# Optimization experiments

Measured on AMD Instinct MI355X. Metric: run time of the kernel, lower is better.

The kernel has to match this reference:

```python
import jax, jax.numpy as jnp
import numpy as np

D3D, D2D, DTEXT, DPROJ, SEQ_LEN = 256, 768, 3072, 3072, 256
B, S, T = 32, 256, 512


def setup_inputs() -> dict:
    key = jax.random.key(0)
    ks = jax.random.split(key, 9)
    s3 = 1.0 / np.sqrt(D3D)
    s2 = 1.0 / np.sqrt(D2D)
    sf = 1.0 / np.sqrt(DPROJ * 3)
    return {
        "feat_3d": jax.random.normal(ks[0], (B, D3D), jnp.float32),
        "feat_2d": jax.random.normal(ks[1], (B, S, D2D), jnp.float32),
        "feat_text": jax.random.normal(ks[2], (B, T, DTEXT), jnp.float32),
        "W3d": jax.random.uniform(ks[3], (DPROJ, D3D), jnp.float32, -s3, s3),
        "b3d": jax.random.uniform(ks[4], (DPROJ,), jnp.float32, -s3, s3),
        "W2d": jax.random.uniform(ks[5], (DPROJ, D2D), jnp.float32, -s2, s2),
        "b2d": jax.random.uniform(ks[6], (DPROJ,), jnp.float32, -s2, s2),
        "Wf": jax.random.uniform(ks[7], (DPROJ, DPROJ * 3), jnp.float32, -sf, sf),
        "bf": jax.random.uniform(ks[8], (DPROJ,), jnp.float32, -sf, sf),
    }


def reference(feat_3d, feat_2d, feat_text, W3d, b3d, W2d, b2d, Wf, bf):
    # Projections
    f3p = feat_3d @ W3d.T + b3d                      # [B, P]
    f2p = jnp.einsum("bsd,pd->bsp", feat_2d, W2d) + b2d  # [B, S, P]

    # Attention pooling of 2D slice features against global 3D feature
    scores_s = jnp.einsum("bsp,bp->bs", f2p, f3p)    # [B, S]
    w_s = jax.nn.softmax(scores_s, axis=1)
    pooled_2d = jnp.einsum("bs,bsp->bp", w_s, f2p)   # [B, P]

    # Attention pooling of text features against global 3D feature
    scores_t = jnp.einsum("btp,bp->bt", feat_text, f3p)  # [B, T]
    w_t = jax.nn.softmax(scores_t, axis=1)
    pooled_text = jnp.einsum("bt,btp->bp", w_t, feat_text)  # [B, P]

    # All seq_len rows of the original's concatenated input are identical,
    # so compute the fusion GEMM once per batch element and broadcast.
    fused_vec = jnp.concatenate([f3p, pooled_2d, pooled_text], axis=-1) @ Wf.T + bf  # [B, P]
    return jnp.broadcast_to(fused_vec[:, None, :], (fused_vec.shape[0], SEQ_LEN, fused_vec.shape[1]))
```

## Files before the change

### kernel.cpp

```cpp
#include <hip/hip_runtime.h>

#define NB 32
#define NS 256
#define NT 512
#define KD3 256
#define KD2 768
#define NP 3072
#define KFZ 9216

__device__ __forceinline__ float wave_red_sum(float v) {
#pragma unroll
  for (int o = 32; o; o >>= 1) v += __shfl_xor(v, o, 64);
  return v;
}
__device__ __forceinline__ float wave_red_max(float v) {
#pragma unroll
  for (int o = 32; o; o >>= 1) v = fmaxf(v, __shfl_xor(v, o, 64));
  return v;
}

__global__ __launch_bounds__(256) void k1_f3p(const float* __restrict__ f3d,
                                              const float* __restrict__ W3d,
                                              const float* __restrict__ b3d,
                                              float* __restrict__ c0, float* __restrict__ c1,
                                              float* __restrict__ c2, float* __restrict__ c3) {
  int b = blockIdx.x & 31, pc = blockIdx.x >> 5;
  __shared__ float4 xs[KD3 / 4];
  int tid = threadIdx.x;
  if (tid < KD3 / 4) xs[tid] = ((const float4*)(f3d + b * KD3))[tid];
  __syncthreads();
  int p = pc * 256 + tid;
  const float4* wrow = (const float4*)(W3d + (size_t)p * KD3);
  float acc = b3d[p];
#pragma unroll 8
  for (int i = 0; i < KD3 / 4; ++i) {
    float4 w = wrow[i], x = xs[i];
    acc = fmaf(w.x, x.x, acc); acc = fmaf(w.y, x.y, acc);
    acc = fmaf(w.z, x.z, acc); acc = fmaf(w.w, x.w, acc);
  }
  size_t o = (size_t)b * KFZ + p;
  c0[o] = acc; c1[o] = 0.f; c2[o] = 0.f; c3[o] = 0.f;
}

__global__ __launch_bounds__(256, 2) void kT_text(const float* __restrict__ ftx,
                                                  const float* __restrict__ c0,
                                                  float* __restrict__ Pt,
                                                  float* __restrict__ ml) {
  int b = blockIdx.x & 31, tch = blockIdx.x >> 5;
  __shared__ float4 f4[NP / 4];
  int tid = threadIdx.x;
#pragma unroll
  for (int i = 0; i < 3; ++i)
    f4[tid + 256 * i] = ((const float4*)(c0 + (size_t)b * KFZ))[tid + 256 * i];
  __syncthreads();
  int wave = tid >> 6, lane = tid & 63;
  int t0 = tch * 32 + wave * 8;
  const float4* rbase = (const float4*)(ftx + ((size_t)(b * NT + t0)) * NP);
  float4 xa[12], xb[12];
#pragma unroll
  for (int j = 0; j < 12; ++j) xa[j] = rbase[lane + 64 * j];
  float m = -3.0e38f, l = 0.f;
  float4 acc[12];
#pragma unroll
  for (int j = 0; j < 12; ++j) acc[j] = make_float4(0.f, 0.f, 0.f, 0.f);
#pragma unroll
  for (int r = 0; r < 8; ++r) {
    float4* cur = (r & 1) ? xb : xa;
    float4* nxt = (r & 1) ? xa : xb;
    if (r < 7) {
      const float4* rn = rbase + (size_t)(r + 1) * (NP / 4);
#pragma unroll
      for (int j = 0; j < 12; ++j) nxt[j] = rn[lane + 64 * j];
    }
    float sx = 0.f, sy = 0.f, sz = 0.f, sw = 0.f;
#pragma unroll
    for (int j = 0; j < 12; ++j) {
      float4 f = f4[lane + 64 * j];
      sx = fmaf(cur[j].x, f.x, sx); sy = fmaf(cur[j].y, f.y, sy);
      sz = fmaf(cur[j].z, f.z, sz); sw = fmaf(cur[j].w, f.w, sw);
    }
    float s = (sx + sy) + (sz + sw);
    s = wave_red_sum(s);
    float mn = fmaxf(m, s);
    float al = __expf(m - mn);
    float e = __expf(s - mn);
    l = fmaf(l, al, e);
#pragma unroll
    for (int j = 0; j < 12; ++j) {
      acc[j].x = fmaf(acc[j].x, al, e * cur[j].x);
      acc[j].y = fmaf(acc[j].y, al, e * cur[j].y);
      acc[j].z = fmaf(acc[j].z, al, e * cur[j].z);
      acc[j].w = fmaf(acc[j].w, al, e * cur[j].w);
    }
    m = mn;
  }
  int c = tch * 4 + wave;
  float4* Pr = (float4*)(Pt + (size_t)(c * NB + b) * NP);
#pragma unroll
  for (int j = 0; j < 12; ++j) Pr[lane + 64 * j] = acc[j];
  if (lane == 0) { ml[(c * NB + b) * 2] = m; ml[(c * NB + b) * 2 + 1] = l; }
}

__global__ __launch_bounds__(256) void k2_gpart(const float* __restrict__ W2d,
                                                const float* __restrict__ c0,
                                                float* __restrict__ g_part) {
  int dc = blockIdx.x % 3, kc = blockIdx.x / 3;
  __shared__ float xs[NB * 96];
  int tid = threadIdx.x;
  int p0 = kc * 96;
  for (int i = tid; i < NB * 96; i += 256) {
    int bb = i / 96, pp = i - bb * 96;
    xs[i] = c0[(size_t)bb * KFZ + p0 + pp];
  }
  __syncthreads();
  int d = dc * 256 + tid;
  float acc[NB];
#pragma unroll
  for (int b = 0; b < NB; ++b) acc[b] = 0.f;
  for (int pp = 0; pp < 96; pp += 8) {
    float w[8];
#pragma unroll
    for (int u = 0; u < 8; ++u) w[u] = W2d[(size_t)(p0 + pp + u) * KD2 + d];
#pragma unroll
    for (int b = 0; b < NB; ++b) {
      float4 x0 = *(const float4*)&xs[b * 96 + pp];
      float4 x1 = *(const float4*)&xs[b * 96 + pp + 4];
      acc[b] = fmaf(w[0], x0.x, acc[b]); acc[b] = fmaf(w[1], x0.y, acc[b]);
      acc[b] = fmaf(w[2], x0.z, acc[b]); acc[b] = fmaf(w[3], x0.w, acc[b]);
      acc[b] = fmaf(w[4], x1.x, acc[b]); acc[b] = fmaf(w[5], x1.y, acc[b]);
      acc[b] = fmaf(w[6], x1.z, acc[b]); acc[b] = fmaf(w[7], x1.w, acc[b]);
    }
  }
#pragma unroll
  for (int b = 0; b < NB; ++b) g_part[(size_t)(kc * NB + b) * KD2 + d] = acc[b];
}

__global__ __launch_bounds__(256) void k3a_scores(const float* __restrict__ f2d,
                                                  const float* __restrict__ g_part,
                                                  float* __restrict__ sraw) {
  int b = blockIdx.x & 31, sc = blockIdx.x >> 5;
  __shared__ float4 g4[KD2 / 4];
  float* g = (float*)g4;
  int tid = threadIdx.x;
  for (int i = tid; i < KD2; i += 256) {
    float a = 0.f;
#pragma unroll 8
    for (int c = 0; c < 32; ++c) a += g_part[(size_t)(c * NB + b) * KD2 + i];
    g[i] = a;
  }
  __syncthreads();
  int wave = tid >> 6, lane = tid & 63;
#pragma unroll
  for (int grp = 0; grp < 2; ++grp) {
    int s0 = sc * 32 + wave * 8 + grp * 4;
    float4 x[4][3];
#pragma unroll
    for (int rr = 0; rr < 4; ++rr) {
      const float4* row = (const float4*)(f2d + ((size_t)b * NS + s0 + rr) * KD2);
#pragma unroll
      for (int j = 0; j < 3; ++j) x[rr][j] = row[lane + 64 * j];
    }
#pragma unroll
    for (int rr = 0; rr < 4; ++rr) {
      float acc = 0.f;
#pragma unroll
      for (int j = 0; j < 3; ++j) {
        float4 f = g4[lane + 64 * j];
        acc = fmaf(x[rr][j].x, f.x, acc); acc = fmaf(x[rr][j].y, f.y, acc);
        acc = fmaf(x[rr][j].z, f.z, acc); acc = fmaf(x[rr][j].w, f.w, acc);
      }
      acc = wave_red_sum(acc);
      if (lane == 0) sraw[b * NS + s0 + rr] = acc;
    }
  }
}

__global__ __launch_bounds__(256) void kComb(const float* __restrict__ Pt,
                                             const float* __restrict__ ml,
                                             float* __restrict__ c0, float* __restrict__ c1,
                                             float* __restrict__ c2, float* __restrict__ c3) {
  int b = blockIdx.x & 31, pc = blockIdx.x >> 5;
  __shared__ float sm[128];
  int tid = threadIdx.x;
  if (tid < 64) {
    sm[tid] = ml[(tid * NB + b) * 2];
    sm[64 + tid] = ml[(tid * NB + b) * 2 + 1];
  }
  __syncthreads();
  float M = -3.0e38f;
#pragma unroll 8
  for (int c = 0; c < 64; ++c) M = fmaxf(M, sm[c]);
  float denom = 0.f;
#pragma unroll 8
  for (int c = 0; c < 64; ++c) denom += __expf(sm[c] - M) * sm[64 + c];
  float inv = 1.f / denom;
  int p4 = pc * 1024 + tid * 4;
  float4 a = make_float4(0.f, 0.f, 0.f, 0.f);
#pragma unroll 2
  for (int cg = 0; cg < 8; ++cg) {
    float4 v[8];
#pragma unroll
    for (int u = 0; u < 8; ++u)
      v[u] = *(const float4*)&Pt[(size_t)((cg * 8 + u) * NB + b) * NP + p4];
#pragma unroll
    for (int u = 0; u < 8; ++u) {
      float w = __expf(sm[cg * 8 + u] - M);
      a.x = fmaf(w, v[u].x, a.x); a.y = fmaf(w, v[u].y, a.y);
      a.z = fmaf(w, v[u].z, a.z); a.w = fmaf(w, v[u].w, a.w);
    }
  }
  a.x *= inv; a.y *= inv; a.z *= inv; a.w *= inv;
  size_t o = (size_t)b * KFZ + 2 * NP + p4;
  float4 z = make_float4(0.f, 0.f, 0.f, 0.f);
  *(float4*)&c0[o] = a;
  *(float4*)&c1[o] = z; *(float4*)&c2[o] = z; *(float4*)&c3[o] = z;
}

__global__ __launch_bounds__(256) void k3c_sm(const float* __restrict__ f2d,
                                              const float* __restrict__ sraw,
                                              float* __restrict__ p2f) {
  int b = blockIdx.x & 31;
  int r = blockIdx.x >> 5;
  int dc = r % 3, sc = r / 3;
  __shared__ float pr[NS];
  __shared__ float red[8];
  int tid = threadIdx.x;
  int wave = tid >> 6, lane = tid & 63;
  float v = sraw[b * NS + tid];
  float mx = wave_red_max(v);
  if (lane == 0) red[wave] = mx;
  __syncthreads();
  float M = fmaxf(fmaxf(red[0], red[1]), fmaxf(red[2], red[3]));
  float e = __expf(v - M);
  pr[tid] = e;
  float smv = wave_red_sum(e);
  if (lane == 0) red[4 + wave] = smv;
  __syncthreads();
  float inv = 1.f / (red[4] + red[5] + red[6] + red[7]);
  int d = dc * 256 + tid;
  float acc = 0.f;
  const float* base = f2d + ((size_t)b * NS + sc * 64) * KD2 + d;
#pragma unroll 2
  for (int sg = 0; sg < 8; ++sg) {
    float xv[8];
#pragma unroll
    for (int u = 0; u < 8; ++u) xv[u] = base[(size_t)(sg * 8 + u) * KD2];
#pragma unroll
    for (int u = 0; u < 8; ++u) acc = fmaf(pr[sc * 64 + sg * 8 + u], xv[u], acc);
  }
  p2f[(size_t)(sc * NB + b) * KD2 + d] = acc * inv;
}

__global__ __launch_bounds__(256) void k5_pool2d(const float* __restrict__ W2d,
                                                 const float* __restrict__ b2d,
                                                 const float* __restrict__ p2f,
                                                 float* __restrict__ c0, float* __restrict__ c1,
                                                 float* __restrict__ c2, float* __restrict__ c3) {
  int pb = blockIdx.x >> 2, ks = blockIdx.x & 3;
  __shared__ __align__(16) float wt[64 * 68];
  __shared__ __align__(16) float xt[32 * 68];
  int tid = threadIdx.x;
  int tp = tid & 31, tb = tid >> 5;
  float acc[2][4];
#pragma unroll
  for (int i = 0; i < 2; ++i)
#pragma unroll
    for (int j = 0; j < 4; ++j) acc[i][j] = 0.f;
  for (int dk = 0; dk < 3; ++dk) {
    int d0 = ks * 192 + dk * 64;
#pragma unroll
    for (int it = 0; it < 4; ++it) {
      int idx = tid + it * 256;
      int row = idx >> 4, c4 = (idx & 15) * 4;
      *(float4*)&wt[row * 68 + c4] =
          *(const float4*)&W2d[(size_t)(pb * 64 + row) * KD2 + d0 + c4];
    }
#pragma unroll
    for (int it = 0; it < 2; ++it) {
      int idx = tid + it * 256;
      int row = idx >> 4, c4 = (idx & 15) * 4;
      float4 a = *(const float4*)&p2f[(size_t)row * KD2 + d0 + c4];
      float4 q1 = *(const float4*)&p2f[(size_t)(NB + row) * KD2 + d0 + c4];
      float4 q2 = *(const float4*)&p2f[(size_t)(2 * NB + row) * KD2 + d0 + c4];
      float4 q3 = *(const float4*)&p2f[(size_t)(3 * NB + row) * KD2 + d0 + c4];
      a.x += q1.x + q2.x + q3.x; a.y += q1.y + q2.y + q3.y;
      a.z += q1.z + q2.z + q3.z; a.w += q1.w + q2.w + q3.w;
      *(float4*)&xt[row * 68 + c4] = a;
    }
    __syncthreads();
#pragma unroll 4
    for (int kk = 0; kk < 64; kk += 4) {
      float4 wv[2], xv[4];
#pragma unroll
      for (int i = 0; i < 2; ++i) wv[i] = *(const float4*)&wt[(tp + 32 * i) * 68 + kk];
#pragma unroll
      for (int j = 0; j < 4; ++j) xv[j] = *(const float4*)&xt[(tb + 8 * j) * 68 + kk];
#pragma unroll
      for (int i = 0; i < 2; ++i)
#pragma unroll
        for (int j = 0; j < 4; ++j) {
          acc[i][j] = fmaf(wv[i].x, xv[j].x, acc[i][j]);
          acc[i][j] = fmaf(wv[i].y, xv[j].y, acc[i][j]);
          acc[i][j] = fmaf(wv[i].z, xv[j].z, acc[i][j]);
          acc[i][j] = fmaf(wv[i].w, xv[j].w, acc[i][j]);
        }
    }
    __syncthreads();
  }
  float* dst = (ks == 0) ? c0 : (ks == 1) ? c1 : (ks == 2) ? c2 : c3;
#pragma unroll
  for (int i = 0; i < 2; ++i) {
    int p = pb * 64 + tp + 32 * i;
    float bias = (ks == 0) ? b2d[p] : 0.f;
#pragma unroll
    for (int j = 0; j < 4; ++j)
      dst[(size_t)(tb + 8 * j) * KFZ + NP + p] = acc[i][j] + bias;
  }
}

__global__ __launch_bounds__(256) void k_csum(float* __restrict__ c0,
                                              const float* __restrict__ c1,
                                              const float* __restrict__ c2,
                                              const float* __restrict__ c3) {
  int i = blockIdx.x * 256 + threadIdx.x;
  float4 a = ((float4*)c0)[i];
  float4 v1 = ((const float4*)c1)[i];
  float4 v2 = ((const float4*)c2)[i];
  float4 v3 = ((const float4*)c3)[i];
  a.x += v1.x + v2.x + v3.x; a.y += v1.y + v2.y + v3.y;
  a.z += v1.z + v2.z + v3.z; a.w += v1.w + v2.w + v3.w;
  ((float4*)c0)[i] = a;
}

__global__ __launch_bounds__(256) void k6_fused(const float* __restrict__ Wf,
                                                const float* __restrict__ c0,
                                                float* __restrict__ fpart) {
  int pb = blockIdx.x >> 4, kc = blockIdx.x & 15;
  __shared__ __align__(16) float wt[96 * 68];
  __shared__ __align__(16) float xt[32 * 68];
  int tid = threadIdx.x;
  int tp = tid & 31, tb = tid >> 5;
  float acc[3][4];
#pragma unroll
  for (int i = 0; i < 3; ++i)
#pragma unroll
    for (int j = 0; j < 4; ++j) acc[i][j] = 0.f;
  for (int kt = 0; kt < 9; ++kt) {
    int k0 = kc * 576 + kt * 64;
#pragma unroll
    for (int it = 0; it < 6; ++it) {
      int idx = tid + it * 256;
      int row = idx >> 4, c4 = (idx & 15) * 4;
      *(float4*)&wt[row * 68 + c4] =
          *(const float4*)&Wf[(size_t)(pb * 96 + row) * KFZ + k0 + c4];
    }
#pragma unroll
    for (int it = 0; it < 2; ++it) {
      int idx = tid + it * 256;
      int row = idx >> 4, c4 = (idx & 15) * 4;
      *(float4*)&xt[row * 68 + c4] =
          *(const float4*)&c0[(size_t)row * KFZ + k0 + c4];
    }
    __syncthreads();
#pragma unroll 4
    for (int kk = 0; kk < 64; kk += 4) {
      float4 wv[3], xv[4];
#pragma unroll
      for (int i = 0; i < 3; ++i) wv[i] = *(const float4*)&wt[(tp + 32 * i) * 68 + kk];
#pragma unroll
      for (int j = 0; j < 4; ++j) xv[j] = *(const float4*)&xt[(tb + 8 * j) * 68 + kk];
#pragma unroll
      for (int i = 0; i < 3; ++i)
#pragma unroll
        for (int j = 0; j < 4; ++j) {
          acc[i][j] = fmaf(wv[i].x, xv[j].x, acc[i][j]);
          acc[i][j] = fmaf(wv[i].y, xv[j].y, acc[i][j]);
          acc[i][j] = fmaf(wv[i].z, xv[j].z, acc[i][j]);
          acc[i][j] = fmaf(wv[i].w, xv[j].w, acc[i][j]);
        }
    }
    __syncthreads();
  }
#pragma unroll
  for (int i = 0; i < 3; ++i)
#pragma unroll
    for (int j = 0; j < 4; ++j)
      fpart[(size_t)(kc * NB + tb + 8 * j) * NP + pb * 96 + tp + 32 * i] = acc[i][j];
}

__global__ __launch_bounds__(256) void k7_bcast(const float* __restrict__ fpart,
                                                const float* __restrict__ bfv,
                                                float* __restrict__ out) {
  int b = blockIdx.x & 31;
  int r = blockIdx.x >> 5;
  int pc = r % 3, sc = r / 3;
  int tid = threadIdx.x;
  int p4 = pc * 1024 + 4 * tid;
  float4 v = *(const float4*)&bfv[p4];
#pragma unroll
  for (int c = 0; c < 16; ++c) {
    float4 a = *(const float4*)&fpart[(size_t)(c * NB + b) * NP + p4];
    v.x += a.x; v.y += a.y; v.z += a.z; v.w += a.w;
  }
  float* obase = out + (size_t)b * NS * NP + p4;
#pragma unroll 4
  for (int ss = 0; ss < 32; ++ss) {
    int s = sc * 32 + ss;
    *(float4*)(obase + (size_t)s * NP) = v;
  }
}

extern "C" void kernel_launch(void* const* d_in, const int* in_sizes, int n_in,
                              void* d_out, int out_size, void* d_ws, size_t ws_size,
                              hipStream_t stream) {
  const float* f3d = (const float*)d_in[0];
  const float* f2d = (const float*)d_in[1];
  const float* ftx = (const float*)d_in[2];
  const float* W3d = (const float*)d_in[3];
  const float* b3d = (const float*)d_in[4];
  const float* W2d = (const float*)d_in[5];
  const float* b2d = (const float*)d_in[6];
  const float* Wf  = (const float*)d_in[7];
  const float* bfv = (const float*)d_in[8];
  float* out = (float*)d_out;
  float* ws = (float*)d_ws;

  float* c0     = ws;
  float* c1     = ws + 294912;
  float* c2     = ws + 589824;
  float* c3     = ws + 884736;
  float* g_part = ws + 1179648;
  float* sraw   = ws + 1966080;
  float* p2f    = ws + 1974272;
  float* ml     = ws + 2072576;
  float* Pt     = ws + 2076672;
  float* fpart  = ws + 8368128;

  k1_f3p<<<384, 256, 0, stream>>>(f3d, W3d, b3d, c0, c1, c2, c3);
  kT_text<<<512, 256, 0, stream>>>(ftx, c0, Pt, ml);
  k2_gpart<<<96, 256, 0, stream>>>(W2d, c0, g_part);
  k3a_scores<<<256, 256, 0, stream>>>(f2d, g_part, sraw);
  kComb<<<96, 256, 0, stream>>>(Pt, ml, c0, c1, c2, c3);
  k3c_sm<<<384, 256, 0, stream>>>(f2d, sraw, p2f);
  k5_pool2d<<<192, 256, 0, stream>>>(W2d, b2d, p2f, c0, c1, c2, c3);
  k_csum<<<288, 256, 0, stream>>>(c0, c1, c2, c3);
  k6_fused<<<512, 256, 0, stream>>>(Wf, c0, fpart);
  k7_bcast<<<768, 256, 0, stream>>>(fpart, bfv, out);
}
```

Baseline: 539.8 us.

## Retile fusion GEMM with register blocking, double-buffered LDS and wider split-K

The fusion GEMM kernel now uses 256 blocks, each covering 768 output columns by all 32 batch rows with a 12x8 register tile per thread. LDS is double-buffered and the global loads for the next K slice are issued while the current one is computed. Split-K widens from 16 to 64 chunks. The broadcast kernel now reduces the 64 partials and, with only 96 blocks, each block writes all 256 sequence rows. The aim is more arithmetic per LDS read and better overlap of loads with math. In exchange the partial buffer grows fourfold and the large output write is spread over far fewer blocks, which may leave much of the GPU idle during that write.

```diff
diff --git a/kernel.cpp b/kernel.cpp
--- a/kernel.cpp
+++ b/kernel.cpp
@@ -332,82 +332,94 @@
   ((float4*)c0)[i] = a;
 }
 
-__global__ __launch_bounds__(256) void k6_fused(const float* __restrict__ Wf,
-                                                const float* __restrict__ c0,
-                                                float* __restrict__ fpart) {
-  int pb = blockIdx.x >> 4, kc = blockIdx.x & 15;
-  __shared__ __align__(16) float wt[96 * 68];
-  __shared__ __align__(16) float xt[32 * 68];
-  int tid = threadIdx.x;
-  int tp = tid & 31, tb = tid >> 5;
-  float acc[3][4];
-#pragma unroll
-  for (int i = 0; i < 3; ++i)
-#pragma unroll
-    for (int j = 0; j < 4; ++j) acc[i][j] = 0.f;
-  for (int kt = 0; kt < 9; ++kt) {
-    int k0 = kc * 576 + kt * 64;
-#pragma unroll
-    for (int it = 0; it < 6; ++it) {
-      int idx = tid + it * 256;
-      int row = idx >> 4, c4 = (idx & 15) * 4;
-      *(float4*)&wt[row * 68 + c4] =
-          *(const float4*)&Wf[(size_t)(pb * 96 + row) * KFZ + k0 + c4];
-    }
-#pragma unroll
-    for (int it = 0; it < 2; ++it) {
-      int idx = tid + it * 256;
-      int row = idx >> 4, c4 = (idx & 15) * 4;
-      *(float4*)&xt[row * 68 + c4] =
-          *(const float4*)&c0[(size_t)row * KFZ + k0 + c4];
-    }
-    __syncthreads();
-#pragma unroll 4
-    for (int kk = 0; kk < 64; kk += 4) {
-      float4 wv[3], xv[4];
-#pragma unroll
-      for (int i = 0; i < 3; ++i) wv[i] = *(const float4*)&wt[(tp + 32 * i) * 68 + kk];
-#pragma unroll
-      for (int j = 0; j < 4; ++j) xv[j] = *(const float4*)&xt[(tb + 8 * j) * 68 + kk];
-#pragma unroll
-      for (int i = 0; i < 3; ++i)
-#pragma unroll
-        for (int j = 0; j < 4; ++j) {
-          acc[i][j] = fmaf(wv[i].x, xv[j].x, acc[i][j]);
-          acc[i][j] = fmaf(wv[i].y, xv[j].y, acc[i][j]);
-          acc[i][j] = fmaf(wv[i].z, xv[j].z, acc[i][j]);
-          acc[i][j] = fmaf(wv[i].w, xv[j].w, acc[i][j]);
+__global__ __launch_bounds__(256, 1) void k6_fused(const float* __restrict__ Wf,
+                                                   const float* __restrict__ c0,
+                                                   float* __restrict__ fpart) {
+  int pb = blockIdx.x & 3, kc = blockIdx.x >> 2;
+  __shared__ float4 wt[2][4 * 768];
+  __shared__ float4 xt[2][128];
+  int tid = threadIdx.x;
+  int wave = tid >> 6, lane = tid & 63;
+  int p0g = pb * 768;
+  int k00 = kc * 144;
+
+  float acc[12][8];
+#pragma unroll
+  for (int i = 0; i < 12; ++i)
+#pragma unroll
+    for (int j = 0; j < 8; ++j) acc[i][j] = 0.f;
+
+  float4 st[12];
+  float4 xst;
+  int xb = tid & 31, xk = tid >> 5;
+
+  auto LOADS = [&](int t) {
+    int k0 = k00 + t * 16;
+#pragma unroll
+    for (int it = 0; it < 12; ++it)
+      st[it] = *(const float4*)&Wf[(size_t)(p0g + it * 64 + lane) * KFZ + k0 + wave * 4];
+    if (tid < 128)
+      xst = *(const float4*)&c0[(size_t)xb * KFZ + k0 + xk * 4];
+  };
+  auto WRITES = [&](int buf) {
+#pragma unroll
+    for (int it = 0; it < 12; ++it) wt[buf][wave * 768 + it * 64 + lane] = st[it];
+    if (tid < 128) xt[buf][tid] = xst;
+  };
+
+  LOADS(0);
+  WRITES(0);
+  __syncthreads();
+  for (int t = 0; t < 9; ++t) {
+    int buf = t & 1;
+    if (t < 8) LOADS(t + 1);
+#pragma unroll
+    for (int s = 0; s < 4; ++s) {
+      float4 xv[8];
+#pragma unroll
+      for (int j = 0; j < 8; ++j) xv[j] = xt[buf][s * 32 + wave * 8 + j];
+#pragma unroll
+      for (int i = 0; i < 12; ++i) {
+        float4 wv = wt[buf][s * 768 + i * 64 + lane];
+#pragma unroll
+        for (int j = 0; j < 8; ++j) {
+          acc[i][j] = fmaf(wv.x, xv[j].x, acc[i][j]);
+          acc[i][j] = fmaf(wv.y, xv[j].y, acc[i][j]);
+          acc[i][j] = fmaf(wv.z, xv[j].z, acc[i][j]);
+          acc[i][j] = fmaf(wv.w, xv[j].w, acc[i][j]);
         }
-    }
-    __syncthreads();
-  }
-#pragma unroll
-  for (int i = 0; i < 3; ++i)
-#pragma unroll
-    for (int j = 0; j < 4; ++j)
-      fpart[(size_t)(kc * NB + tb + 8 * j) * NP + pb * 96 + tp + 32 * i] = acc[i][j];
+      }
+    }
+    if (t < 8) {
+      WRITES(buf ^ 1);
+      __syncthreads();
+    }
+  }
+  float* fb = fpart + (size_t)(kc * NB + wave * 8) * NP + p0g + lane;
+#pragma unroll
+  for (int j = 0; j < 8; ++j)
+#pragma unroll
+    for (int i = 0; i < 12; ++i)
+      fb[(size_t)j * NP + i * 64] = acc[i][j];
 }
 
 __global__ __launch_bounds__(256) void k7_bcast(const float* __restrict__ fpart,
                                                 const float* __restrict__ bfv,
                                                 float* __restrict__ out) {
   int b = blockIdx.x & 31;
-  int r = blockIdx.x >> 5;
-  int pc = r % 3, sc = r / 3;
+  int pc = blockIdx.x >> 5;
   int tid = threadIdx.x;
   int p4 = pc * 1024 + 4 * tid;
   float4 v = *(const float4*)&bfv[p4];
-#pragma unroll
-  for (int c = 0; c < 16; ++c) {
+#pragma unroll 8
+  for (int c = 0; c < 64; ++c) {
     float4 a = *(const float4*)&fpart[(size_t)(c * NB + b) * NP + p4];
     v.x += a.x; v.y += a.y; v.z += a.z; v.w += a.w;
   }
   float* obase = out + (size_t)b * NS * NP + p4;
 #pragma unroll 4
-  for (int ss = 0; ss < 32; ++ss) {
-    int s = sc * 32 + ss;
+  for (int s = 0; s < NS; ++s)
     *(float4*)(obase + (size_t)s * NP) = v;
-  }
 }
 
 extern "C" void kernel_launch(void* const* d_in, const int* in_sizes, int n_in,
@@ -444,6 +456,6 @@
   k3c_sm<<<384, 256, 0, stream>>>(f2d, sraw, p2f);
   k5_pool2d<<<192, 256, 0, stream>>>(W2d, b2d, p2f, c0, c1, c2, c3);
   k_csum<<<288, 256, 0, stream>>>(c0, c1, c2, c3);
-  k6_fused<<<512, 256, 0, stream>>>(Wf, c0, fpart);
-  k7_bcast<<<768, 256, 0, stream>>>(fpart, bfv, out);
-}
+  k6_fused<<<256, 256, 0, stream>>>(Wf, c0, fpart);
+  k7_bcast<<<96, 256, 0, stream>>>(fpart, bfv, out);
+}
```

Result: slower. 610.5 us (+13.1%).
